# Kernel optimization log

Hardware: AMD Instinct MI355X
Metric: run time of the kernel (lower is better)

Reference implementation:

```python
import jax, jax.numpy as jnp
import numpy as np

# Graph / model dims (match init_kwargs config)
N1, N2, N3 = 80000, 16000, 4096
E1, E2 = 256000, 65536
D_IN, H1, C1 = 256, 8, 64   # conv1: concat -> 512
H2, C2 = 4, 64              # conv2: mean over heads -> gnn_outdim=64
F_IN, F_HID, L_DIM, N_CLS = 128, 64, 64, 1


def setup_inputs() -> dict:
    key = jax.random.key(0)
    ks = jax.random.split(key, 20)
    rng = np.random.default_rng(0)

    def edges(E, n_src, n_dst):
        src = rng.integers(0, n_src, size=E)
        dst = rng.integers(0, n_dst, size=E)
        # avoid incidental self loops (PyG remove_self_loops); explicit ones added in conv
        src = np.where(src == dst, src + 1, src)
        return jnp.asarray(src, jnp.int32), jnp.asarray(dst, jnp.int32)

    es1, ed1 = edges(E1, N1, N2)
    es2, ed2 = edges(E2, N2, N3)
    s = 0.05
    return {
        "x": jax.random.normal(ks[0], (N1, D_IN), jnp.float32),
        "flat": jax.random.normal(ks[1], (N3, F_IN), jnp.float32),
        "last": jax.random.normal(ks[2], (N3, L_DIM), jnp.float32),
        "edge_src1": es1, "edge_dst1": ed1,
        "edge_src2": es2, "edge_dst2": ed2,
        "W1_src": jax.random.normal(ks[3], (D_IN, H1 * C1), jnp.float32) * s,
        "W1_dst": jax.random.normal(ks[4], (D_IN, H1 * C1), jnp.float32) * s,
        "att1_src": jax.random.normal(ks[5], (H1, C1), jnp.float32) * s,
        "att1_dst": jax.random.normal(ks[6], (H1, C1), jnp.float32) * s,
        "bias1": jax.random.normal(ks[7], (H1 * C1,), jnp.float32) * s,
        "W2_src": jax.random.normal(ks[8], (H1 * C1, H2 * C2), jnp.float32) * s,
        "W2_dst": jax.random.normal(ks[9], (H1 * C1, H2 * C2), jnp.float32) * s,
        "att2_src": jax.random.normal(ks[10], (H2, C2), jnp.float32) * s,
        "att2_dst": jax.random.normal(ks[11], (H2, C2), jnp.float32) * s,
        "bias2": jax.random.normal(ks[12], (C2,), jnp.float32) * s,
        "flat_W": jax.random.normal(ks[13], (F_IN, F_HID), jnp.float32) * s,
        "flat_b": jax.random.normal(ks[14], (F_HID,), jnp.float32) * s,
        "out_W": jax.random.normal(ks[15], (C2 + F_HID + L_DIM, N_CLS), jnp.float32) * s,
        "out_b": jax.random.normal(ks[16], (N_CLS,), jnp.float32) * s,
    }


def gat_conv(x_src, x_dst, src, dst, W_s, W_d, a_s, a_d, b, concat):
    """PyG bipartite GATConv (eval mode, add_self_loops=True, neg slope 0.2)."""
    H, C = a_s.shape
    Ns, Nd = x_src.shape[0], x_dst.shape[0]
    h_s = (x_src @ W_s).reshape(Ns, H, C)
    h_d = (x_dst @ W_d).reshape(Nd, H, C)
    sl = jnp.arange(Nd, dtype=src.dtype)
    src = jnp.concatenate([src, sl])  # self loops on target nodes
    dst = jnp.concatenate([dst, sl])
    e_s = jnp.einsum("nhc,hc->nh", h_s, a_s)  # [Ns,H]
    e_d = jnp.einsum("nhc,hc->nh", h_d, a_d)  # [Nd,H]
    alpha = jax.nn.leaky_relu(e_s[src] + e_d[dst], negative_slope=0.2)  # [E,H]
    amax = jax.ops.segment_max(alpha, dst, num_segments=Nd)[dst]
    ex = jnp.exp(alpha - amax)
    w = ex / jax.ops.segment_sum(ex, dst, num_segments=Nd)[dst]  # segment softmax
    msg = w[:, :, None] * h_s[src]  # [E,H,C]
    out = jax.ops.segment_sum(msg, dst, num_segments=Nd)  # [Nd,H,C]
    out = out.reshape(Nd, H * C) if concat else out.mean(axis=1)
    return out + b


def reference(x, flat, last, edge_src1, edge_dst1, edge_src2, edge_dst2,
              W1_src, W1_dst, att1_src, att1_dst, bias1,
              W2_src, W2_dst, att2_src, att2_dst, bias2,
              flat_W, flat_b, out_W, out_b):
    # eval mode: featdrop / attndrop / main_dropout are identity
    h = gat_conv(x, x[:N2], edge_src1, edge_dst1,
                 W1_src, W1_dst, att1_src, att1_dst, bias1, concat=True)
    h = jax.nn.elu(h)
    h = gat_conv(h, h[:N3], edge_src2, edge_dst2,
                 W2_src, W2_dst, att2_src, att2_dst, bias2, concat=False)
    f = flat @ flat_W + flat_b
    z = jnp.concatenate([h, f, last], axis=1)  # [N3, 64+64+64]
    return z @ out_W + out_b  # [N3, num_cls]
```

## Files before the change

### kernel.cpp

```cpp
#include <hip/hip_runtime.h>
#include <hip/hip_bf16.h>
#include <cstdio>

typedef __attribute__((ext_vector_type(8))) short short8;
typedef __attribute__((ext_vector_type(4))) short short4v;
typedef __attribute__((ext_vector_type(8))) _Float16 half8;
typedef __attribute__((ext_vector_type(4))) float f32x4;

template <int H> struct VecT;
template <> struct VecT<8> { using T = short8; };
template <> struct VecT<4> { using T = short4v; };

__device__ __forceinline__ float bfu2f(unsigned short u) {
    return __uint_as_float(((unsigned)u) << 16);
}
__device__ __forceinline__ unsigned short f2bfu(float f) {
    __hip_bfloat16 b = __float2bfloat16(f);
    union { __hip_bfloat16 b; unsigned short u; } cv; cv.b = b;
    return cv.u;
}
__device__ __forceinline__ unsigned short f2hu(float f) {
    _Float16 h = (_Float16)f;
    union { _Float16 h; unsigned short u; } cv; cv.h = h;
    return cv.u;
}

#define N1 80000
#define N2 16000
#define N3 4096
#define E1 256000
#define E2 65536

__global__ void prep_kernel(const float* __restrict__ W1s, const float* __restrict__ W1d,
                            unsigned short* __restrict__ w1s_pk, unsigned short* __restrict__ w1d_pk,
                            const float* __restrict__ W2s, const float* __restrict__ W2d,
                            unsigned short* __restrict__ w2s_pk, unsigned short* __restrict__ w2d_pk,
                            const float* __restrict__ fW, unsigned short* __restrict__ fw_t3,
                            int* __restrict__ zbase, int zn) {
    int i = blockIdx.x * blockDim.x + threadIdx.x;
    const int S0 = 262144, S1 = 262144, S2 = 8192;
    if (i < S0) {
        const float* W = (i < 131072) ? W1s : W1d;
        unsigned short* pk = (i < 131072) ? w1s_pk : w1d_pk;
        int j = i & 131071;
        int k = j >> 9, n = j & 511;
        int n16 = n >> 4, l = n & 15, k32 = k >> 5, qq = (k >> 3) & 3, e = k & 7;
        size_t base = ((size_t)(n16 * 8 + k32)) * 512 + (qq * 16 + l) * 8 + e;
        pk[base] = f2hu(W[j]);
    } else if (i < S0 + S1) {
        int ii = i - S0;
        const float* W = (ii < 131072) ? W2s : W2d;
        unsigned short* pk = (ii < 131072) ? w2s_pk : w2d_pk;
        int j = ii & 131071;
        int k = j >> 8, n = j & 255;
        int n16 = n >> 4, l = n & 15, k32 = k >> 5, qq = (k >> 3) & 3, e = k & 7;
        size_t base = ((size_t)(n16 * 16 + k32)) * 512 + (qq * 16 + l) * 8 + e;
        pk[base] = f2hu(W[j]);
    } else if (i < S0 + S1 + S2) {
        int j = i - S0 - S1;
        int k = j >> 6, n = j & 63;
        float v = fW[j];
        unsigned short h = f2bfu(v);
        unsigned short l = f2bfu(v - bfu2f(h));
        size_t base = (size_t)n * 384;
        fw_t3[base + k] = h;
        fw_t3[base + 128 + k] = l;
        fw_t3[base + 256 + k] = h;
    } else {
        int j = i - S0 - S1 - S2;
        if (j < zn) zbase[j] = 0;
    }
}

__global__ void hist_dual(const int* __restrict__ d1, int* __restrict__ c1,
                          const int* __restrict__ d2, int* __restrict__ c2) {
    int i = blockIdx.x * blockDim.x + threadIdx.x;
    if (i < E1) {
        int d = d1[i];
        if ((unsigned)d < (unsigned)N2) atomicAdd(&c1[d], 1);
    } else if (i < E1 + E2) {
        int d = d2[i - E1];
        if ((unsigned)d < (unsigned)N3) atomicAdd(&c2[d], 1);
    }
}
__global__ __launch_bounds__(1024)
void scan_dual(const int* __restrict__ c1, int* __restrict__ s1, int Nd1,
               const int* __restrict__ c2, int* __restrict__ s2, int Nd2) {
    const int* cnt = (blockIdx.x == 0) ? c1 : c2;
    int* start = (blockIdx.x == 0) ? s1 : s2;
    int Nd = (blockIdx.x == 0) ? Nd1 : Nd2;
    __shared__ int part[1024];
    int t = threadIdx.x;
    int k = (Nd + 1023) >> 10;
    int lo = t * k, hi = min(lo + k, Nd);
    if (lo > Nd) lo = Nd;
    int s = 0;
    for (int i = lo; i < hi; i++) s += cnt[i];
    part[t] = s;
    __syncthreads();
    for (int off = 1; off < 1024; off <<= 1) {
        int v = (t >= off) ? part[t - off] : 0;
        __syncthreads();
        part[t] += v;
        __syncthreads();
    }
    int run = (t > 0) ? part[t - 1] : 0;
    for (int i = lo; i < hi; i++) { start[i] = run; run += cnt[i]; }
    if (t == 1023) start[Nd] = part[1023];
}
__global__ void fill_dual(const int* __restrict__ sa1, const int* __restrict__ da1,
                          const int* __restrict__ st1, int* __restrict__ cu1, int* __restrict__ cs1,
                          const int* __restrict__ sa2, const int* __restrict__ da2,
                          const int* __restrict__ st2, int* __restrict__ cu2, int* __restrict__ cs2) {
    int i = blockIdx.x * blockDim.x + threadIdx.x;
    const int *sa, *da, *st;
    int *cu, *cs;
    int Nd, Ns, e;
    if (i < E1) { sa = sa1; da = da1; st = st1; cu = cu1; cs = cs1; Nd = N2; Ns = N1; e = i; }
    else if (i < E1 + E2) { sa = sa2; da = da2; st = st2; cu = cu2; cs = cs2; Nd = N3; Ns = N2; e = i - E1; }
    else return;
    int d = da[e];
    if ((unsigned)d >= (unsigned)Nd) return;
    int p = atomicAdd(&cu[d], 1);
    int idx = st[d] + p;
    if (idx >= st[d + 1]) return;
    int s = sa[e];
    if ((unsigned)s >= (unsigned)Ns) s = 0;
    cs[idx] = s;
}

template <bool AF16>
__global__ __launch_bounds__(256, 2)
void gemm_lds(const void* __restrict__ Ax,
              const unsigned short* __restrict__ Bp1, unsigned short* __restrict__ C1,
              const float* __restrict__ att1, float* __restrict__ es1,
              const unsigned short* __restrict__ Bp2, unsigned short* __restrict__ C2,
              const float* __restrict__ att2, float* __restrict__ es2,
              int Mb1, int MT, int NB, int N, int K, int H) {
    __shared__ alignas(16) _Float16 As[2][64][40];
    const int hb = blockIdx.x;
    const int xcd = hb & 7;
    const int sI = hb >> 3;
    const int mt = (sI / NB) * 8 + xcd;
    const int nb = sI % NB;
    if (mt >= MT) return;
    const unsigned short* Bp; unsigned short* C; const float* att; float* es_out;
    int m0;
    if (mt < Mb1) { Bp = Bp1; C = C1; att = att1; es_out = es1; m0 = mt * 64; }
    else          { Bp = Bp2; C = C2; att = att2; es_out = es2; m0 = (mt - Mb1) * 64; }
    const int tid = threadIdx.x;
    const int wave = tid >> 6, lane = tid & 63;
    const int q = lane >> 4, l15 = lane & 15;
    const int n0 = nb * 256 + wave * 64;
    const int KS = K >> 5;
    const int arow = tid >> 2, ac8 = (tid & 3) * 8;
    const unsigned short* Bbase = Bp + (size_t)(n0 >> 4) * KS * 512 + lane * 8;

    f32x4 acc[4][4] = {};
    half8 b[4];
    float4 s0, s1;
    half8 sh;

    auto stageLoad = [&](int t) {
        if constexpr (AF16) {
            const _Float16* p = (const _Float16*)Ax + (size_t)(m0 + arow) * K + t * 32 + ac8;
            sh = *(const half8*)p;
        } else {
            const float* p = (const float*)Ax + (size_t)(m0 + arow) * K + t * 32 + ac8;
            s0 = *(const float4*)p;
            s1 = *(const float4*)(p + 4);
        }
    };
    auto stageWrite = [&](int buf) {
        half8 v;
        if constexpr (AF16) {
            v = sh;
        } else {
            v[0] = (_Float16)s0.x; v[1] = (_Float16)s0.y;
            v[2] = (_Float16)s0.z; v[3] = (_Float16)s0.w;
            v[4] = (_Float16)s1.x; v[5] = (_Float16)s1.y;
            v[6] = (_Float16)s1.z; v[7] = (_Float16)s1.w;
        }
        *(half8*)&As[buf][arow][ac8] = v;
    };
    auto loadB = [&](int k32, int nt) {
        b[nt] = *(const half8*)(Bbase + ((size_t)nt * KS + k32) * 512);
    };

    stageLoad(0);
#pragma unroll
    for (int nt = 0; nt < 4; nt++) loadB(0, nt);
    stageWrite(0);
    __syncthreads();

    int cur = 0;
    for (int t = 0; t < KS; t++) {
        const bool hn = (t + 1) < KS;
        if (hn) stageLoad(t + 1);
#pragma unroll
        for (int rg = 0; rg < 4; rg++) {
            half8 a = *(const half8*)&As[cur][rg * 16 + l15][q * 8];
#pragma unroll
            for (int nt = 0; nt < 4; nt++) {
                acc[rg][nt] = __builtin_amdgcn_mfma_f32_16x16x32_f16(a, b[nt], acc[rg][nt], 0, 0, 0);
                if (rg == 3 && hn) loadB(t + 1, nt);
            }
        }
        if (hn) {
            stageWrite(cur ^ 1);
            __syncthreads();
        }
        cur ^= 1;
    }

#pragma unroll
    for (int rg = 0; rg < 4; rg++)
#pragma unroll
        for (int nt = 0; nt < 4; nt++)
#pragma unroll
            for (int r = 0; r < 4; r++) {
                int row = m0 + rg * 16 + q * 4 + r;
                int col = n0 + nt * 16 + l15;
                C[(size_t)row * N + col] = f2bfu(acc[rg][nt][r]);
            }
    {
        const int head = n0 >> 6;
        float av[4];
#pragma unroll
        for (int nt = 0; nt < 4; nt++) av[nt] = att[head * 64 + nt * 16 + l15];
#pragma unroll
        for (int rg = 0; rg < 4; rg++)
#pragma unroll
            for (int r = 0; r < 4; r++) {
                float p = acc[rg][0][r] * av[0] + acc[rg][1][r] * av[1]
                        + acc[rg][2][r] * av[2] + acc[rg][3][r] * av[3];
#pragma unroll
                for (int off = 1; off < 16; off <<= 1) p += __shfl_xor(p, off);
                if (l15 == 0)
                    es_out[(size_t)(m0 + rg * 16 + q * 4 + r) * H + head] = p;
            }
    }
}

__global__ __launch_bounds__(256)
void gemm_mfma(const float* __restrict__ A, const unsigned short* __restrict__ Bt3,
               float* __restrict__ C, int M, int N, int K) {
    const int KK = 3 * K;
    __shared__ unsigned short As[2][64][72];
    __shared__ unsigned short Bs[64][72];
    const int tid = threadIdx.x;
    const int wave = tid >> 6, lane = tid & 63;
    const int wr = wave >> 1, wc = wave & 1;
    const int quad = lane >> 4, l15 = lane & 15;
    const int m0 = blockIdx.y * 64, n0 = blockIdx.x * 64;
    f32x4 acc[2][2] = {};
    for (int k0 = 0; k0 < KK; k0 += 64) {
        const int seg = k0 / K;
        const int ks = k0 - seg * K;
#pragma unroll
        for (int i = 0; i < 2; i++) {
            int idx = tid + i * 256;
            int r = idx >> 3, cv = (idx & 7) * 8;
            const float* ap = &A[(size_t)(m0 + r) * K + ks + cv];
            const float4 v0 = *(const float4*)ap;
            const float4 v1 = *(const float4*)(ap + 4);
            float va[8] = {v0.x, v0.y, v0.z, v0.w, v1.x, v1.y, v1.z, v1.w};
            short8 h8, l8;
#pragma unroll
            for (int j = 0; j < 8; j++) {
                unsigned short hh = f2bfu(va[j]);
                h8[j] = (short)hh;
                l8[j] = (short)f2bfu(va[j] - bfu2f(hh));
            }
            *(short8*)&As[0][r][cv] = h8;
            *(short8*)&As[1][r][cv] = l8;
            *(short8*)&Bs[r][cv] = *(const short8*)&Bt3[(size_t)(n0 + r) * KK + k0 + cv];
        }
        __syncthreads();
        const int abank = (seg < 2) ? 0 : 1;
#pragma unroll
        for (int kk = 0; kk < 64; kk += 32) {
            short8 a[2], b[2];
#pragma unroll
            for (int t = 0; t < 2; t++) {
                a[t] = *(const short8*)&As[abank][wr * 32 + t * 16 + l15][kk + quad * 8];
                b[t] = *(const short8*)&Bs[wc * 32 + t * 16 + l15][kk + quad * 8];
            }
#pragma unroll
            for (int mt = 0; mt < 2; mt++)
#pragma unroll
                for (int nt = 0; nt < 2; nt++)
                    acc[mt][nt] = __builtin_amdgcn_mfma_f32_16x16x32_bf16(
                        a[mt], b[nt], acc[mt][nt], 0, 0, 0);
        }
        __syncthreads();
    }
#pragma unroll
    for (int mt = 0; mt < 2; mt++)
#pragma unroll
        for (int nt = 0; nt < 2; nt++)
#pragma unroll
            for (int r = 0; r < 4; r++) {
                int row = m0 + wr * 32 + mt * 16 + quad * 4 + r;
                int col = n0 + wc * 32 + nt * 16 + l15;
                C[(size_t)row * N + col] = acc[mt][nt][r];
            }
}

template <int H, bool ELU, bool HOUT>
__global__ __launch_bounds__(256)
void gat_agg2(const int* __restrict__ csr, const int* __restrict__ rs,
              const unsigned short* __restrict__ hs,
              const float* __restrict__ es,
              const float* __restrict__ ed,
              const float* __restrict__ bias,
              void* __restrict__ out,
              int Nd) {
    constexpr int LH = (H == 8) ? 3 : 2;
    constexpr int EPC = 64 >> LH;
    const int lane = threadIdx.x & 63;
    const int d = blockIdx.x * (blockDim.x >> 6) + (threadIdx.x >> 6);
    if (d >= Nd) return;
    const int beg = rs[d];
    const int deg = rs[d + 1] - beg;
    const int n = deg + 1;
    const int h = lane & (H - 1);
    const int e0 = lane >> LH;
    const float edh = ed[(size_t)d * H + h];
    float mx = -1e30f;
    for (int j0 = 0; j0 < n; j0 += EPC) {
        int j = j0 + e0;
        if (j < n) {
            int s = (j < deg) ? csr[beg + j] : d;
            float a = es[(size_t)s * H + h] + edh;
            a = (a > 0.0f) ? a : 0.2f * a;
            mx = fmaxf(mx, a);
        }
    }
#pragma unroll
    for (int off = H; off < 64; off <<= 1) mx = fmaxf(mx, __shfl_xor(mx, off));
    float den = 0.0f;
    for (int j0 = 0; j0 < n; j0 += EPC) {
        int j = j0 + e0;
        if (j < n) {
            int s = (j < deg) ? csr[beg + j] : d;
            float a = es[(size_t)s * H + h] + edh;
            a = (a > 0.0f) ? a : 0.2f * a;
            den += expf(a - mx);
        }
    }
#pragma unroll
    for (int off = H; off < 64; off <<= 1) den += __shfl_xor(den, off);
    const float inv = 1.0f / den;
    const int hB = lane >> (6 - LH);
    const float mB = __shfl(mx, hB);
    const float invB = __shfl(inv, hB);
    const float edhB = __shfl(edh, hB);
    using V = typename VecT<H>::T;
    float acc[H] = {};
    const size_t rowoff = (size_t)lane * H;
    int j = 0;
    for (; j + 4 <= n; j += 4) {
        int s[4]; V rv[4]; float w[4];
#pragma unroll
        for (int u = 0; u < 4; u++) { int jj = j + u; s[u] = (jj < deg) ? csr[beg + jj] : d; }
#pragma unroll
        for (int u = 0; u < 4; u++) rv[u] = *(const V*)&hs[(size_t)s[u] * (H * 64) + rowoff];
#pragma unroll
        for (int u = 0; u < 4; u++) {
            float a = es[(size_t)s[u] * H + hB] + edhB;
            a = (a > 0.0f) ? a : 0.2f * a;
            w[u] = expf(a - mB) * invB;
        }
#pragma unroll
        for (int u = 0; u < 4; u++)
#pragma unroll
            for (int k = 0; k < H; k++) acc[k] += w[u] * bfu2f((unsigned short)rv[u][k]);
    }
    for (; j < n; j++) {
        int s = (j < deg) ? csr[beg + j] : d;
        V rv = *(const V*)&hs[(size_t)s * (H * 64) + rowoff];
        float a = es[(size_t)s * H + hB] + edhB;
        a = (a > 0.0f) ? a : 0.2f * a;
        float w = expf(a - mB) * invB;
#pragma unroll
        for (int k = 0; k < H; k++) acc[k] += w * bfu2f((unsigned short)rv[k]);
    }
#pragma unroll
    for (int k = 0; k < H; k++) {
        float v = acc[k];
        if (ELU) {
            v += bias[lane * H + k];
            v = (v > 0.0f) ? v : expm1f(v);
        }
        acc[k] = v;
    }
    if constexpr (HOUT) {
        half8 hv;
#pragma unroll
        for (int k = 0; k < H; k++) hv[k] = (_Float16)acc[k];
        _Float16* op = (_Float16*)out + (size_t)d * (H * 64) + rowoff;
        *(half8*)op = hv;
    } else {
        float* op = (float*)out + (size_t)d * (H * 64) + rowoff;
#pragma unroll
        for (int qd = 0; qd < H / 4; qd++)
            *(float4*)&op[qd * 4] = *(float4*)&acc[qd * 4];
    }
}

__global__ void final_kernel(const float* __restrict__ acc2, const float* __restrict__ bias2,
                             const float* __restrict__ fbuf, const float* __restrict__ flat_b,
                             const float* __restrict__ last, const float* __restrict__ outW,
                             const float* __restrict__ outb, float* __restrict__ out, int N) {
    int n = blockIdx.x * blockDim.x + threadIdx.x;
    if (n >= N) return;
    float s = outb[0];
    const float* a = acc2 + (size_t)n * 256;
    for (int c = 0; c < 64; c++) {
        float h2 = 0.25f * (a[c] + a[64 + c] + a[128 + c] + a[192 + c]) + bias2[c];
        s += h2 * outW[c];
        s += (fbuf[(size_t)n * 64 + c] + flat_b[c]) * outW[64 + c];
        s += last[(size_t)n * 64 + c] * outW[128 + c];
    }
    out[n] = s;
}

extern "C" void kernel_launch(void* const* d_in, const int* in_sizes, int n_in,
                              void* d_out, int out_size, void* d_ws, size_t ws_size,
                              hipStream_t stream) {
    const float* x    = (const float*)d_in[0];
    const float* flat = (const float*)d_in[1];
    const float* last = (const float*)d_in[2];
    const int*  es1i  = (const int*)d_in[3];
    const int*  ed1i  = (const int*)d_in[4];
    const int*  es2i  = (const int*)d_in[5];
    const int*  ed2i  = (const int*)d_in[6];
    const float* W1s  = (const float*)d_in[7];
    const float* W1d  = (const float*)d_in[8];
    const float* a1s  = (const float*)d_in[9];
    const float* a1d  = (const float*)d_in[10];
    const float* b1   = (const float*)d_in[11];
    const float* W2s  = (const float*)d_in[12];
    const float* W2d  = (const float*)d_in[13];
    const float* a2s  = (const float*)d_in[14];
    const float* a2d  = (const float*)d_in[15];
    const float* b2   = (const float*)d_in[16];
    const float* fW   = (const float*)d_in[17];
    const float* fb   = (const float*)d_in[18];
    const float* oW   = (const float*)d_in[19];
    const float* ob   = (const float*)d_in[20];
    float* out = (float*)d_out;

    float* ws = (float*)d_ws;
    unsigned short* hs1_bf = (unsigned short*)ws;
    unsigned short* hd1_bf = (unsigned short*)(ws + 20480000);
    float* es1f = ws + 24576000;
    float* ed1f = ws + 25216000;
    float* acc1 = ws + 25344000;
    unsigned short* wb = (unsigned short*)(ws + 54016000);
    unsigned short* w1s_pk = wb;
    unsigned short* w1d_pk = wb + 262144;
    unsigned short* w2s_pk = wb + 524288;
    unsigned short* w2d_pk = wb + 786432;
    unsigned short* fw_t3  = wb + 1048576;
    int* ibase   = (int*)(ws + 54816000);
    int* cnt1    = ibase;
    int* cursor1 = ibase + 16000;
    int* cnt2    = ibase + 32000;
    int* cursor2 = ibase + 36096;
    int* start1  = ibase + 40192;
    int* start2  = ibase + 56193;
    int* csr1    = ibase + 60290;
    int* csr2    = ibase + 316290;
    const size_t NEED = ((size_t)54816000 + 381826) * 4;
    if (ws_size < NEED) {
        fprintf(stderr, "kernel_launch: ws_size %zu < needed %zu\n", ws_size, NEED);
        return;
    }
    unsigned short* hs2_bf = (unsigned short*)ws;
    unsigned short* hd2_bf = (unsigned short*)(ws + 2048000);
    float* es2f = ws + 2572288;
    float* ed2f = ws + 2636288;
    float* acc2 = ws + 2652672;
    float* fbuf = ws + 3701248;
    unsigned short* acc1h = (unsigned short*)acc1;

    {
        int total = 262144 + 262144 + 8192 + 40192;
        prep_kernel<<<(total + 255) / 256, 256, 0, stream>>>(
            W1s, W1d, w1s_pk, w1d_pk,
            W2s, W2d, w2s_pk, w2d_pk,
            fW, fw_t3, ibase, 40192);
    }
    hist_dual<<<(E1 + E2 + 255) / 256, 256, 0, stream>>>(ed1i, cnt1, ed2i, cnt2);
    scan_dual<<<2, 1024, 0, stream>>>(cnt1, start1, N2, cnt2, start2, N3);
    fill_dual<<<(E1 + E2 + 255) / 256, 256, 0, stream>>>(
        es1i, ed1i, start1, cursor1, csr1, es2i, ed2i, start2, cursor2, csr2);

    {
        const int MT = N1 / 64 + N2 / 64;
        const int NB = 512 / 256;
        const int grid = 8 * NB * ((MT + 7) / 8);
        gemm_lds<false><<<grid, 256, 0, stream>>>(
            x, w1s_pk, hs1_bf, a1s, es1f,
            w1d_pk, hd1_bf, a1d, ed1f,
            N1 / 64, MT, NB, 512, 256, 8);
    }
    gat_agg2<8, true, true><<<N2 / 4, 256, 0, stream>>>(
        csr1, start1, hs1_bf, es1f, ed1f, b1, acc1h, N2);

    {
        const int MT = N2 / 64 + N3 / 64;
        const int NB = 1;
        const int grid = 8 * NB * ((MT + 7) / 8);
        gemm_lds<true><<<grid, 256, 0, stream>>>(
            acc1h, w2s_pk, hs2_bf, a2s, es2f,
            w2d_pk, hd2_bf, a2d, ed2f,
            N2 / 64, MT, NB, 256, 512, 4);
    }
    gat_agg2<4, false, false><<<N3 / 4, 256, 0, stream>>>(
        csr2, start2, hs2_bf, es2f, ed2f, nullptr, acc2, N3);

    gemm_mfma<<<dim3(1, N3 / 64), 256, 0, stream>>>(flat, fw_t3, fbuf, N3, 64, 128);
    final_kernel<<<(N3 + 255) / 256, 256, 0, stream>>>(acc2, b2, fbuf, fb, last, oW, ob, out, N3);
}
```

Measured before the change: 381.5 us.

## Widen GEMM K-step to 64, cache softmax logits, unroll aggregation by 8

The LDS-staged GEMM now processes 64 K elements per stage instead of 32, with two B register sets, which halves the number of barriers and LDS buffer swaps. In the GAT aggregation kernel, nodes with small degree keep their attention logits in registers so the second pass skips reloading csr/es, and the gather loop gains an 8-wide unrolled stage for more memory-level parallelism. The cost is higher register pressure in both kernels, which may reduce occupancy.

New measurement: 379.2 us. About the same (-0.6%).

```diff
diff --git a/kernel.cpp b/kernel.cpp
--- a/kernel.cpp
+++ b/kernel.cpp
@@ -137,7 +137,7 @@
               const unsigned short* __restrict__ Bp2, unsigned short* __restrict__ C2,
               const float* __restrict__ att2, float* __restrict__ es2,
               int Mb1, int MT, int NB, int N, int K, int H) {
-    __shared__ alignas(16) _Float16 As[2][64][40];
+    __shared__ alignas(16) _Float16 As[2][64][72];
     const int hb = blockIdx.x;
     const int xcd = hb & 7;
     const int sI = hb >> 3;
@@ -152,44 +152,55 @@
     const int wave = tid >> 6, lane = tid & 63;
     const int q = lane >> 4, l15 = lane & 15;
     const int n0 = nb * 256 + wave * 64;
-    const int KS = K >> 5;
-    const int arow = tid >> 2, ac8 = (tid & 3) * 8;
-    const unsigned short* Bbase = Bp + (size_t)(n0 >> 4) * KS * 512 + lane * 8;
+    const int KS = K >> 6;
+    const int KSB = K >> 5;
+    const int arow = tid >> 2, ac16 = (tid & 3) * 16;
+    const unsigned short* Bbase = Bp + (size_t)(n0 >> 4) * KSB * 512 + lane * 8;
 
     f32x4 acc[4][4] = {};
-    half8 b[4];
-    float4 s0, s1;
-    half8 sh;
+    half8 b[2][4];
+    float4 s0, s1, s2, s3;
+    half8 sh0, sh1;
 
     auto stageLoad = [&](int t) {
         if constexpr (AF16) {
-            const _Float16* p = (const _Float16*)Ax + (size_t)(m0 + arow) * K + t * 32 + ac8;
-            sh = *(const half8*)p;
+            const _Float16* p = (const _Float16*)Ax + (size_t)(m0 + arow) * K + t * 64 + ac16;
+            sh0 = *(const half8*)p;
+            sh1 = *(const half8*)(p + 8);
         } else {
-            const float* p = (const float*)Ax + (size_t)(m0 + arow) * K + t * 32 + ac8;
+            const float* p = (const float*)Ax + (size_t)(m0 + arow) * K + t * 64 + ac16;
             s0 = *(const float4*)p;
             s1 = *(const float4*)(p + 4);
+            s2 = *(const float4*)(p + 8);
+            s3 = *(const float4*)(p + 12);
         }
     };
     auto stageWrite = [&](int buf) {
-        half8 v;
+        half8 v0, v1;
         if constexpr (AF16) {
-            v = sh;
+            v0 = sh0; v1 = sh1;
         } else {
-            v[0] = (_Float16)s0.x; v[1] = (_Float16)s0.y;
-            v[2] = (_Float16)s0.z; v[3] = (_Float16)s0.w;
-            v[4] = (_Float16)s1.x; v[5] = (_Float16)s1.y;
-            v[6] = (_Float16)s1.z; v[7] = (_Float16)s1.w;
-        }
-        *(half8*)&As[buf][arow][ac8] = v;
+            v0[0] = (_Float16)s0.x; v0[1] = (_Float16)s0.y;
+            v0[2] = (_Float16)s0.z; v0[3] = (_Float16)s0.w;
+            v0[4] = (_Float16)s1.x; v0[5] = (_Float16)s1.y;
+            v0[6] = (_Float16)s1.z; v0[7] = (_Float16)s1.w;
+            v1[0] = (_Float16)s2.x; v1[1] = (_Float16)s2.y;
+            v1[2] = (_Float16)s2.z; v1[3] = (_Float16)s2.w;
+            v1[4] = (_Float16)s3.x; v1[5] = (_Float16)s3.y;
+            v1[6] = (_Float16)s3.z; v1[7] = (_Float16)s3.w;
+        }
+        *(half8*)&As[buf][arow][ac16] = v0;
+        *(half8*)&As[buf][arow][ac16 + 8] = v1;
     };
-    auto loadB = [&](int k32, int nt) {
-        b[nt] = *(const half8*)(Bbase + ((size_t)nt * KS + k32) * 512);
+    auto loadB = [&](int k32, int kh, int nt) {
+        b[kh][nt] = *(const half8*)(Bbase + ((size_t)nt * KSB + k32) * 512);
     };
 
     stageLoad(0);
 #pragma unroll
-    for (int nt = 0; nt < 4; nt++) loadB(0, nt);
+    for (int kh = 0; kh < 2; kh++)
+#pragma unroll
+        for (int nt = 0; nt < 4; nt++) loadB(kh, kh, nt);
     stageWrite(0);
     __syncthreads();
 
@@ -198,12 +209,15 @@
         const bool hn = (t + 1) < KS;
         if (hn) stageLoad(t + 1);
 #pragma unroll
-        for (int rg = 0; rg < 4; rg++) {
-            half8 a = *(const half8*)&As[cur][rg * 16 + l15][q * 8];
-#pragma unroll
-            for (int nt = 0; nt < 4; nt++) {
-                acc[rg][nt] = __builtin_amdgcn_mfma_f32_16x16x32_f16(a, b[nt], acc[rg][nt], 0, 0, 0);
-                if (rg == 3 && hn) loadB(t + 1, nt);
+        for (int kh = 0; kh < 2; kh++) {
+#pragma unroll
+            for (int rg = 0; rg < 4; rg++) {
+                half8 a = *(const half8*)&As[cur][rg * 16 + l15][kh * 32 + q * 8];
+#pragma unroll
+                for (int nt = 0; nt < 4; nt++) {
+                    acc[rg][nt] = __builtin_amdgcn_mfma_f32_16x16x32_f16(a, b[kh][nt], acc[rg][nt], 0, 0, 0);
+                    if (rg == 3 && hn) loadB(2 * (t + 1) + kh, kh, nt);
+                }
             }
         }
         if (hn) {
@@ -327,30 +341,56 @@
     const int h = lane & (H - 1);
     const int e0 = lane >> LH;
     const float edh = ed[(size_t)d * H + h];
+    const int nch = (n + EPC - 1) / EPC;
     float mx = -1e30f;
-    for (int j0 = 0; j0 < n; j0 += EPC) {
-        int j = j0 + e0;
-        if (j < n) {
-            int s = (j < deg) ? csr[beg + j] : d;
-            float a = es[(size_t)s * H + h] + edh;
-            a = (a > 0.0f) ? a : 0.2f * a;
+    float den = 0.0f;
+    if (nch <= 8) {
+        float ac[8];
+#pragma unroll
+        for (int c = 0; c < 8; c++) {
+            float a = -1e30f;
+            if (c < nch) {
+                int j = c * EPC + e0;
+                if (j < n) {
+                    int s = (j < deg) ? csr[beg + j] : d;
+                    a = es[(size_t)s * H + h] + edh;
+                    a = (a > 0.0f) ? a : 0.2f * a;
+                }
+            }
+            ac[c] = a;
             mx = fmaxf(mx, a);
         }
-    }
-#pragma unroll
-    for (int off = H; off < 64; off <<= 1) mx = fmaxf(mx, __shfl_xor(mx, off));
-    float den = 0.0f;
-    for (int j0 = 0; j0 < n; j0 += EPC) {
-        int j = j0 + e0;
-        if (j < n) {
-            int s = (j < deg) ? csr[beg + j] : d;
-            float a = es[(size_t)s * H + h] + edh;
-            a = (a > 0.0f) ? a : 0.2f * a;
-            den += expf(a - mx);
-        }
-    }
-#pragma unroll
-    for (int off = H; off < 64; off <<= 1) den += __shfl_xor(den, off);
+#pragma unroll
+        for (int off = H; off < 64; off <<= 1) mx = fmaxf(mx, __shfl_xor(mx, off));
+#pragma unroll
+        for (int c = 0; c < 8; c++)
+            if (c < nch) den += expf(ac[c] - mx);
+#pragma unroll
+        for (int off = H; off < 64; off <<= 1) den += __shfl_xor(den, off);
+    } else {
+        for (int j0 = 0; j0 < n; j0 += EPC) {
+            int j = j0 + e0;
+            if (j < n) {
+                int s = (j < deg) ? csr[beg + j] : d;
+                float a = es[(size_t)s * H + h] + edh;
+                a = (a > 0.0f) ? a : 0.2f * a;
+                mx = fmaxf(mx, a);
+            }
+        }
+#pragma unroll
+        for (int off = H; off < 64; off <<= 1) mx = fmaxf(mx, __shfl_xor(mx, off));
+        for (int j0 = 0; j0 < n; j0 += EPC) {
+            int j = j0 + e0;
+            if (j < n) {
+                int s = (j < deg) ? csr[beg + j] : d;
+                float a = es[(size_t)s * H + h] + edh;
+                a = (a > 0.0f) ? a : 0.2f * a;
+                den += expf(a - mx);
+            }
+        }
+#pragma unroll
+        for (int off = H; off < 64; off <<= 1) den += __shfl_xor(den, off);
+    }
     const float inv = 1.0f / den;
     const int hB = lane >> (6 - LH);
     const float mB = __shfl(mx, hB);
@@ -360,6 +400,23 @@
     float acc[H] = {};
     const size_t rowoff = (size_t)lane * H;
     int j = 0;
+    for (; j + 8 <= n; j += 8) {
+        int s[8]; V rv[8]; float w[8];
+#pragma unroll
+        for (int u = 0; u < 8; u++) { int jj = j + u; s[u] = (jj < deg) ? csr[beg + jj] : d; }
+#pragma unroll
+        for (int u = 0; u < 8; u++) rv[u] = *(const V*)&hs[(size_t)s[u] * (H * 64) + rowoff];
+#pragma unroll
+        for (int u = 0; u < 8; u++) {
+            float a = es[(size_t)s[u] * H + hB] + edhB;
+            a = (a > 0.0f) ? a : 0.2f * a;
+            w[u] = expf(a - mB) * invB;
+        }
+#pragma unroll
+        for (int u = 0; u < 8; u++)
+#pragma unroll
+            for (int k = 0; k < H; k++) acc[k] += w[u] * bfu2f((unsigned short)rv[u][k]);
+    }
     for (; j + 4 <= n; j += 4) {
         int s[4]; V rv[4]; float w[4];
 #pragma unroll
```
